# Optimization experiments

Hardware: AMD Instinct MI355X
Metric: run time of the kernel (lower is better)

## Reference

```python
import jax, jax.numpy as jnp
import numpy as np

DIM = 64
KSZ = 3


def _conv2d(x, w, b):
    # x: (N, C, H, W), w: (O, I, 3, 3), 'same' padding
    y = jax.lax.conv_general_dilated(
        x, w, window_strides=(1, 1), padding=[(1, 1), (1, 1)],
        dimension_numbers=("NCHW", "OIHW", "NCHW"))
    return y + b[None, :, None, None]


def setup_inputs() -> dict:
    key = jax.random.key(0)
    k1, k2, k3, k4, k5 = jax.random.split(key, 5)
    b, c, t, h, w = 2, DIM, 5, 128, 128
    x = jax.random.normal(k1, (b, c, t, h, w), dtype=jnp.float32)
    # Conv3d kernels have temporal extent 1 -> equivalent 2D kernels
    w1 = jax.random.normal(k2, (DIM, DIM, 3, 3), dtype=jnp.float32) * 0.05
    b1 = jax.random.normal(k3, (DIM,), dtype=jnp.float32) * 0.05
    w2 = jax.random.normal(k4, (KSZ * KSZ, DIM, 3, 3), dtype=jnp.float32) * 0.05
    b2 = jax.random.normal(k5, (KSZ * KSZ,), dtype=jnp.float32) * 0.05
    return {"x": x, "w1": w1, "b1": b1, "w2": w2, "b2": b2}


def reference(x, w1, b1, w2, b2):
    b, c, t, h, w = x.shape
    k = KSZ
    K = t * k * k
    # Conv3d with (1,3,3) kernel == 2D conv applied per frame
    xf = x.transpose(0, 2, 1, 3, 4).reshape(b * t, c, h, w)  # (bt, c, h, w)
    y = _conv2d(xf, w1, b1)
    y = jnp.where(y >= 0, y, 0.2 * y)  # LeakyReLU(0.2)
    ker = _conv2d(y, w2, b2)  # (bt, k*k, h, w)
    # rearrange 'b (k1 k2) t h w -> b h w (t k1 k2)'
    ker = ker.reshape(b, t, k * k, h, w).transpose(0, 3, 4, 1, 2).reshape(b, h, w, K)
    ker = ker[:, None]  # (b, 1, h, w, K)
    # kernel_normalize over last dim
    ker = ker - jnp.mean(ker, axis=-1, keepdims=True) + 1.0 / K
    # replicate pad + unfold (gather kxk neighborhoods)
    pad = (k - 1) // 2
    xp = jnp.pad(xf, ((0, 0), (0, 0), (pad, pad), (pad, pad)), mode="edge")
    patches = jnp.stack(
        [xp[:, :, i:i + h, j:j + w] for i in range(k) for j in range(k)],
        axis=-1)  # (bt, c, h, w, k*k) in (k1,k2) order like F.unfold
    # '(b t) (c k1 k2) (h w) -> b c h w (t k1 k2)'
    patches = patches.reshape(b, t, c, h, w, k * k).transpose(0, 2, 3, 4, 1, 5)
    patches = patches.reshape(b, c, h, w, K)
    return jnp.sum(patches * ker, axis=-1)  # (b, c, h, w)
```

## Files before the change

### kernel.cpp

```cpp
#include <hip/hip_runtime.h>
#include <hip/hip_bf16.h>

#define HH 128
#define WW 128
#define CC 64
#define TT 5
#define HW (HH*WW)
#define NI 10

typedef __attribute__((ext_vector_type(8))) short short8;
typedef __attribute__((ext_vector_type(4))) float f32x4;

__device__ __forceinline__ float bf2f(unsigned int bits16) {
  union { unsigned int u; float f; } v; v.u = bits16 << 16; return v.f;
}
__device__ __forceinline__ unsigned short f2bf(float f) {
  __hip_bfloat16 h = __float2bfloat16(f);
  return *reinterpret_cast<unsigned short*>(&h);
}

__global__ __launch_bounds__(256) void pack_k(const float* __restrict__ x,
    const float* __restrict__ w1, const float* __restrict__ w2,
    unsigned short* __restrict__ xb, unsigned short* __restrict__ wb1,
    unsigned short* __restrict__ wb2) {
  __shared__ unsigned short tb[128*65];
  const int tid = threadIdx.x;
  const int bx = blockIdx.x;
  if (bx >= NI*HH) {
    int idx = (bx - NI*HH)*256 + tid;
    if (idx < 64*576) {
      int oc = idx / 576, rem = idx - oc*576, kk = rem >> 6, ic = rem & 63;
      wb1[idx] = f2bf(w1[(oc*64 + ic)*9 + kk]);
    }
    if (idx < 16*576) {
      int oc = idx / 576, rem = idx - oc*576, kk = rem >> 6, ic = rem & 63;
      wb2[idx] = (oc < 9) ? f2bf(w2[(oc*64 + ic)*9 + kk]) : (unsigned short)0;
    }
    return;
  }
  const int n = bx >> 7, h = bx & 127;
  const int bi = n / 5, ti = n - bi*5;
  const float* xp = x + ((size_t)bi*CC*TT + ti)*HW + (size_t)h*WW;
  for (int e = tid; e < 64*128; e += 256) {
    int ci = e >> 7, w = e & 127;
    tb[w*65 + ci] = f2bf(xp[(size_t)ci*TT*HW + w]);
  }
  __syncthreads();
  unsigned short* dst = xb + ((size_t)n*HW + (size_t)h*WW)*64;
  for (int e = tid; e < 2048; e += 256) {
    int w = e >> 4, c = e & 15;
    *(uint2*)(dst + w*64 + c*4) = *(const uint2*)(&tb[w*65 + c*4]);
  }
}

__global__ __launch_bounds__(256, 2) void conv1_mfma(
    const unsigned short* __restrict__ xb, const unsigned short* __restrict__ wb1,
    const float* __restrict__ b1, unsigned short* __restrict__ yb) {
  __shared__ unsigned short xt[324*64];
  __shared__ unsigned short wt[36*512];
  const int tid = threadIdx.x;
  const int wave = tid >> 6, lane = tid & 63, q = lane >> 4, r = lane & 15;
  const int n = blockIdx.z >> 1, ocg = (blockIdx.z & 1) << 5;
  const int h0 = blockIdx.y << 4, w0 = blockIdx.x << 4;
  const unsigned short* xn = xb + (size_t)n*HW*64;

  {
    const unsigned short* wsrc = wb1 + (size_t)ocg*576;
    for (int e = tid; e < 2304; e += 256) {
      int frag = e >> 6, ln = e & 63;
      int kk = frag >> 2, rem = frag & 3, half = rem >> 1, g = rem & 1;
      *(uint4*)(&wt[e << 3]) = *(const uint4*)(
          wsrc + (size_t)(g*16 + (ln & 15))*576 + kk*64 + half*32 + ((ln >> 4) << 3));
    }
  }
  for (int e = tid; e < 2592; e += 256) {
    int sp = e >> 3, c = e & 7;
    int sr = sp / 18, sc = sp - sr*18;
    int gh = h0 + sr - 1, gw = w0 + sc - 1;
    uint4 v = make_uint4(0u,0u,0u,0u);
    if (gh >= 0 && gh < HH && gw >= 0 && gw < WW)
      v = *(const uint4*)(xn + ((size_t)(gh*WW + gw))*64 + (c << 3));
    *(uint4*)(&xt[sp*64 + ((c ^ (sp & 7)) << 3)]) = v;
  }
  __syncthreads();

  f32x4 zero4 = {0.f, 0.f, 0.f, 0.f};
  f32x4 acc[4][2];
  #pragma unroll
  for (int i = 0; i < 4; ++i)
    #pragma unroll
    for (int g = 0; g < 2; ++g) acc[i][g] = zero4;

  #pragma unroll
  for (int half = 0; half < 2; ++half) {
    short8 bf[6][3];
    #pragma unroll
    for (int rr = 0; rr < 6; ++rr)
      #pragma unroll
      for (int dx = 0; dx < 3; ++dx) {
        int sp = (wave*4 + rr)*18 + (r + dx);
        bf[rr][dx] = *(const short8*)(&xt[sp*64 + ((((half << 2) | q) ^ (sp & 7)) << 3)]);
      }
    #pragma unroll
    for (int kk = 0; kk < 9; ++kk) {
      const int dy = kk / 3, dx = kk - dy*3;
      short8 a0 = *(const short8*)(&wt[((kk*4 + half*2 + 0) << 9) + (lane << 3)]);
      short8 a1 = *(const short8*)(&wt[((kk*4 + half*2 + 1) << 9) + (lane << 3)]);
      #pragma unroll
      for (int i = 0; i < 4; ++i) {
        acc[i][0] = __builtin_amdgcn_mfma_f32_16x16x32_bf16(a0, bf[i+dy][dx], acc[i][0], 0, 0, 0);
        acc[i][1] = __builtin_amdgcn_mfma_f32_16x16x32_bf16(a1, bf[i+dy][dx], acc[i][1], 0, 0, 0);
      }
    }
  }

  #pragma unroll
  for (int i = 0; i < 4; ++i) {
    int py = wave*4 + i;
    unsigned short* yp = yb + ((size_t)n*HW + (h0+py)*WW + (w0+r))*64;
    #pragma unroll
    for (int g = 0; g < 2; ++g) {
      int oc0 = ocg + g*16 + (q << 2);
      f32x4 bias = *(const f32x4*)(b1 + oc0);
      float v0 = acc[i][g][0] + bias[0]; v0 = (v0 >= 0.f) ? v0 : 0.2f*v0;
      float v1 = acc[i][g][1] + bias[1]; v1 = (v1 >= 0.f) ? v1 : 0.2f*v1;
      float v2 = acc[i][g][2] + bias[2]; v2 = (v2 >= 0.f) ? v2 : 0.2f*v2;
      float v3 = acc[i][g][3] + bias[3]; v3 = (v3 >= 0.f) ? v3 : 0.2f*v3;
      uint2 pk;
      pk.x = (unsigned int)f2bf(v0) | ((unsigned int)f2bf(v1) << 16);
      pk.y = (unsigned int)f2bf(v2) | ((unsigned int)f2bf(v3) << 16);
      *(uint2*)(yp + oc0) = pk;
    }
  }
}

__global__ __launch_bounds__(256) void conv2_mfma(
    const unsigned short* __restrict__ yb, const unsigned short* __restrict__ wb2,
    const float* __restrict__ b2, float* __restrict__ ker0) {
  __shared__ unsigned short yt[180*64];
  __shared__ unsigned short wt[18*512];
  const int tid = threadIdx.x;
  const int wave = tid >> 6, lane = tid & 63, q = lane >> 4, r = lane & 15;
  const int n = blockIdx.z;
  const int h0 = blockIdx.y << 3, w0 = blockIdx.x << 4;
  const unsigned short* yn = yb + (size_t)n*HW*64;

  for (int e = tid; e < 1152; e += 256) {
    int frag = e >> 6, ln = e & 63;
    int kk = frag >> 1, half = frag & 1;
    *(uint4*)(&wt[e << 3]) = *(const uint4*)(
        wb2 + (size_t)(ln & 15)*576 + kk*64 + half*32 + ((ln >> 4) << 3));
  }
  for (int e = tid; e < 1440; e += 256) {
    int sp = e >> 3, c = e & 7;
    int sr = sp / 18, sc = sp - sr*18;
    int gh = h0 + sr - 1, gw = w0 + sc - 1;
    uint4 v = make_uint4(0u,0u,0u,0u);
    if (gh >= 0 && gh < HH && gw >= 0 && gw < WW)
      v = *(const uint4*)(yn + ((size_t)(gh*WW + gw))*64 + (c << 3));
    *(uint4*)(&yt[sp*64 + ((c ^ (sp & 7)) << 3)]) = v;
  }
  __syncthreads();

  f32x4 zero4 = {0.f, 0.f, 0.f, 0.f};
  f32x4 acc[2];
  #pragma unroll
  for (int i = 0; i < 2; ++i) acc[i] = zero4;

  #pragma unroll
  for (int half = 0; half < 2; ++half) {
    short8 bf[4][3];
    #pragma unroll
    for (int rr = 0; rr < 4; ++rr)
      #pragma unroll
      for (int dx = 0; dx < 3; ++dx) {
        int sp = (wave*2 + rr)*18 + (r + dx);
        bf[rr][dx] = *(const short8*)(&yt[sp*64 + ((((half << 2) | q) ^ (sp & 7)) << 3)]);
      }
    #pragma unroll
    for (int kk = 0; kk < 9; ++kk) {
      const int dy = kk / 3, dx = kk - dy*3;
      short8 a = *(const short8*)(&wt[((kk*2 + half) << 9) + (lane << 3)]);
      #pragma unroll
      for (int i = 0; i < 2; ++i)
        acc[i] = __builtin_amdgcn_mfma_f32_16x16x32_bf16(a, bf[i+dy][dx], acc[i], 0, 0, 0);
    }
  }

  #pragma unroll
  for (int i = 0; i < 2; ++i) {
    int py = wave*2 + i;
    #pragma unroll
    for (int t2 = 0; t2 < 4; ++t2) {
      int oc = (q << 2) + t2;
      if (oc < 9)
        ker0[((size_t)n*9 + oc)*HW + (h0+py)*WW + w0 + r] = acc[i][t2] + b2[oc];
    }
  }
}

__global__ __launch_bounds__(256) void dynf_k(
    const float* __restrict__ x, const float* __restrict__ ker0,
    float* __restrict__ out) {
  __shared__ float xs[TT*324*4];
  const int tw = threadIdx.x, th = threadIdx.y;
  const int tid = th*16 + tw;
  const int wz = blockIdx.z;
  const int bi = wz >> 4, ci0 = (wz & 15) << 2;
  const int h0 = blockIdx.y << 4, w0 = blockIdx.x << 4;
  const int pix = (h0+th)*WW + w0 + tw;

  float kv[45]; float s = 0.f;
  #pragma unroll
  for (int t5 = 0; t5 < TT; ++t5)
    #pragma unroll
    for (int kk = 0; kk < 9; ++kk) {
      float v = ker0[((size_t)(bi*TT + t5)*9 + kk)*HW + pix];
      kv[t5*9 + kk] = v; s += v;
    }
  const float m = (s - 1.f) * (1.f/45.f);
  #pragma unroll
  for (int qq = 0; qq < 45; ++qq) kv[qq] -= m;

  const float* xc = x + ((size_t)(bi*CC + ci0))*TT*HW;
  for (int e = tid; e < TT*324; e += 256) {
    int t5 = e / 324, sp = e - t5*324;
    int rr = sp / 18, cc = sp - rr*18;
    int gh = min(max(h0 + rr - 1, 0), HH-1);
    int gw = min(max(w0 + cc - 1, 0), WW-1);
    const float* xp = xc + (size_t)t5*HW + gh*WW + gw;
    f32x4 f;
    f[0] = xp[0];
    f[1] = xp[(size_t)TT*HW];
    f[2] = xp[(size_t)2*TT*HW];
    f[3] = xp[(size_t)3*TT*HW];
    *(f32x4*)(&xs[e << 2]) = f;
  }
  __syncthreads();

  float a0 = 0.f, a1 = 0.f, a2 = 0.f, a3 = 0.f;
  #pragma unroll
  for (int t5 = 0; t5 < TT; ++t5)
    #pragma unroll
    for (int dy = 0; dy < 3; ++dy)
      #pragma unroll
      for (int dx = 0; dx < 3; ++dx) {
        f32x4 xv = *(const f32x4*)(&xs[(t5*324 + (th+dy)*18 + (tw+dx)) << 2]);
        float k = kv[t5*9 + dy*3 + dx];
        a0 = fmaf(xv[0], k, a0); a1 = fmaf(xv[1], k, a1);
        a2 = fmaf(xv[2], k, a2); a3 = fmaf(xv[3], k, a3);
      }
  float* op = out + ((size_t)(bi*CC + ci0))*HW + pix;
  op[0] = a0; op[HW] = a1; op[2*(size_t)HW] = a2; op[3*(size_t)HW] = a3;
}

extern "C" void kernel_launch(void* const* d_in, const int* in_sizes, int n_in,
                              void* d_out, int out_size, void* d_ws, size_t ws_size,
                              hipStream_t stream) {
  const float* x  = (const float*)d_in[0];
  const float* w1 = (const float*)d_in[1];
  const float* b1 = (const float*)d_in[2];
  const float* w2 = (const float*)d_in[3];
  const float* b2 = (const float*)d_in[4];
  float* out = (float*)d_out;

  unsigned short* xb  = (unsigned short*)d_ws;
  unsigned short* yb  = xb + (size_t)NI*HW*64;
  float*          ker0 = (float*)(yb + (size_t)NI*HW*64);
  unsigned short* wb1 = (unsigned short*)(ker0 + (size_t)NI*9*HW);
  unsigned short* wb2 = wb1 + 64*576;

  pack_k    <<<NI*HH + 144, 256, 0, stream>>>(x, w1, w2, xb, wb1, wb2);
  conv1_mfma<<<dim3(8,8,2*NI), 256, 0, stream>>>(xb, wb1, b1, yb);
  conv2_mfma<<<dim3(8,16,NI), 256, 0, stream>>>(yb, wb2, b2, ker0);
  dynf_k    <<<dim3(8,8,32), dim3(16,16), 0, stream>>>(x, ker0, out);
}
```

Before: 162.3 us.

## Restructure dynamic filter to reuse per-pixel kernels across all channels from bf16 input

The dynamic-filter kernel now assigns each block an 8x8 pixel tile covering all 64 channels. It loops over 16 rounds of 4 channels, so the 45 normalized per-pixel weights are loaded from ker0 once instead of once per channel group. Input patches now come from the packed channels-last bf16 copy of x rather than the fp32 tensor, which halves the input bytes. The costs are a smaller 10x10 tile with more halo per pixel, 8-byte strided gathers, two barriers per round, fewer blocks in the grid, and bf16 rounding of x in the final weighted sum.

Result: slower. 170.6 us (+5.1%).

```diff
diff --git a/kernel.cpp b/kernel.cpp
--- a/kernel.cpp
+++ b/kernel.cpp
@@ -200,15 +200,15 @@
 }
 
 __global__ __launch_bounds__(256) void dynf_k(
-    const float* __restrict__ x, const float* __restrict__ ker0,
+    const unsigned short* __restrict__ xb, const float* __restrict__ ker0,
     float* __restrict__ out) {
-  __shared__ float xs[TT*324*4];
-  const int tw = threadIdx.x, th = threadIdx.y;
-  const int tid = th*16 + tw;
-  const int wz = blockIdx.z;
-  const int bi = wz >> 4, ci0 = (wz & 15) << 2;
-  const int h0 = blockIdx.y << 4, w0 = blockIdx.x << 4;
-  const int pix = (h0+th)*WW + w0 + tw;
+  __shared__ float xs[TT*100*5];
+  const int tid = threadIdx.x;
+  const int px = tid & 63, cq = tid >> 6;
+  const int pw = px & 7, ph = px >> 3;
+  const int bi = blockIdx.z;
+  const int h0 = blockIdx.y << 3, w0 = blockIdx.x << 3;
+  const int pix = (h0+ph)*WW + w0 + pw;
 
   float kv[45]; float s = 0.f;
   #pragma unroll
@@ -222,36 +222,32 @@
   #pragma unroll
   for (int qq = 0; qq < 45; ++qq) kv[qq] -= m;
 
-  const float* xc = x + ((size_t)(bi*CC + ci0))*TT*HW;
-  for (int e = tid; e < TT*324; e += 256) {
-    int t5 = e / 324, sp = e - t5*324;
-    int rr = sp / 18, cc = sp - rr*18;
-    int gh = min(max(h0 + rr - 1, 0), HH-1);
-    int gw = min(max(w0 + cc - 1, 0), WW-1);
-    const float* xp = xc + (size_t)t5*HW + gh*WW + gw;
-    f32x4 f;
-    f[0] = xp[0];
-    f[1] = xp[(size_t)TT*HW];
-    f[2] = xp[(size_t)2*TT*HW];
-    f[3] = xp[(size_t)3*TT*HW];
-    *(f32x4*)(&xs[e << 2]) = f;
-  }
-  __syncthreads();
-
-  float a0 = 0.f, a1 = 0.f, a2 = 0.f, a3 = 0.f;
-  #pragma unroll
-  for (int t5 = 0; t5 < TT; ++t5)
-    #pragma unroll
-    for (int dy = 0; dy < 3; ++dy)
-      #pragma unroll
-      for (int dx = 0; dx < 3; ++dx) {
-        f32x4 xv = *(const f32x4*)(&xs[(t5*324 + (th+dy)*18 + (tw+dx)) << 2]);
-        float k = kv[t5*9 + dy*3 + dx];
-        a0 = fmaf(xv[0], k, a0); a1 = fmaf(xv[1], k, a1);
-        a2 = fmaf(xv[2], k, a2); a3 = fmaf(xv[3], k, a3);
-      }
-  float* op = out + ((size_t)(bi*CC + ci0))*HW + pix;
-  op[0] = a0; op[HW] = a1; op[2*(size_t)HW] = a2; op[3*(size_t)HW] = a3;
+  for (int rnd = 0; rnd < 16; ++rnd) {
+    __syncthreads();
+    for (int e = tid; e < TT*100; e += 256) {
+      int t5 = e / 100, sp = e - t5*100;
+      int rr2 = sp / 10, cc = sp - rr2*10;
+      int gh = min(max(h0 + rr2 - 1, 0), HH-1);
+      int gw = min(max(w0 + cc - 1, 0), WW-1);
+      uint2 raw = *(const uint2*)(xb + ((size_t)(bi*TT + t5)*HW + gh*WW + gw)*64 + (rnd << 2));
+      float* d = &xs[e*5];
+      d[0] = bf2f(raw.x & 0xffffu);
+      d[1] = bf2f(raw.x >> 16);
+      d[2] = bf2f(raw.y & 0xffffu);
+      d[3] = bf2f(raw.y >> 16);
+    }
+    __syncthreads();
+    float a = 0.f;
+    #pragma unroll
+    for (int t5 = 0; t5 < TT; ++t5)
+      #pragma unroll
+      for (int dy = 0; dy < 3; ++dy)
+        #pragma unroll
+        for (int dx = 0; dx < 3; ++dx)
+          a = fmaf(xs[(t5*100 + (ph+dy)*10 + pw+dx)*5 + cq],
+                   kv[t5*9 + dy*3 + dx], a);
+    out[((size_t)(bi*CC + (rnd << 2) + cq))*HW + pix] = a;
+  }
 }
 
 extern "C" void kernel_launch(void* const* d_in, const int* in_sizes, int n_in,
@@ -273,5 +269,5 @@
   pack_k    <<<NI*HH + 144, 256, 0, stream>>>(x, w1, w2, xb, wb1, wb2);
   conv1_mfma<<<dim3(8,8,2*NI), 256, 0, stream>>>(xb, wb1, b1, yb);
   conv2_mfma<<<dim3(8,16,NI), 256, 0, stream>>>(yb, wb2, b2, ker0);
-  dynf_k    <<<dim3(8,8,32), dim3(16,16), 0, stream>>>(x, ker0, out);
-}
+  dynf_k    <<<dim3(16,16,2), 256, 0, stream>>>(xb, ker0, out);
+}
```
